# Optimization experiments

Hardware: AMD Instinct MI355X
Metric: run time of the kernel (lower is better)

Reference implementation:

```python
import jax, jax.numpy as jnp
import numpy as np

FREQ_DIM = 64
BLOCK_DIM = 64
N = 256          # lattice sites
CH = 6           # channel_num -> block diagonals at offsets -1, 0, +1
S = 2 * 16 + CH - 2   # seq_num = 36
BS = 4           # block_size (kron of two 2x2 matrices)
HID = 128
EPS = 1e-5
B = 32

_e = np.eye(2)
_sx = np.array([[0., 1.], [1., 0.]])
_siy = np.array([[0., 1.], [-1., 0.]])
_sz = np.array([[1., 0.], [0., -1.]])
_p = [_e, _sx, _siy, _sz]
KRONS = jnp.asarray(np.stack([np.kron(_p[a], _p[b]) for a in range(4) for b in range(4)]).astype(np.float32))  # (16,4,4)
Z1 = KRONS[12]  # kron(sigma_z, I) used for interaction blocks ('z1')


def _bn(h, g, b):
    # BatchNorm1d in training mode: biased batch statistics over axis 0
    mu = h.mean(axis=0)
    v = h.var(axis=0)
    return g * (h - mu) / jnp.sqrt(v + EPS) + b


def _mlp(x, Win, bin_, Wmid, bmid, Wout, bout, gamma, beta):
    # depth-4 MLP: Lin+ReLU, then (BN,Lin,ReLU) x2, then BN,Lin,ReLU
    h = jax.nn.relu(x @ Win + bin_)
    for i in range(Wmid.shape[0]):
        h = jax.nn.relu(_bn(h, gamma[i], beta[i]) @ Wmid[i] + bmid[i])
    return jax.nn.relu(_bn(h, gamma[-1], beta[-1]) @ Wout + bout)


def _lstm(xs, h0, c0, Wih, Whh, bih, bhh):
    # xs: (B, T, S); torch gate order i, f, g, o
    def step(carry, x_t):
        h, c = carry
        gates = x_t @ Wih.T + h @ Whh.T + (bih + bhh)
        i, f, g, o = jnp.split(gates, 4, axis=-1)
        c = jax.nn.sigmoid(f) * c + jax.nn.sigmoid(i) * jnp.tanh(g)
        h = jax.nn.sigmoid(o) * jnp.tanh(c)
        return (h, c), h
    _, hs = jax.lax.scan(step, (h0, c0), jnp.swapaxes(xs, 0, 1))
    return jnp.swapaxes(hs, 0, 1)


def setup_inputs() -> dict:
    key = jax.random.key(0)
    ks = iter(jax.random.split(key, 48))
    def w(shape, s=0.05):
        return jax.random.normal(next(ks), shape, dtype=jnp.float32) * s
    d = {
        'x': w((B, FREQ_DIM + BLOCK_DIM), 1.0),
        'fd_Win': w((FREQ_DIM, HID)), 'fd_bin': w((HID,)),
        'fd_Wmid': w((2, HID, HID)), 'fd_bmid': w((2, HID)),
        'fd_Wout': w((HID, S)), 'fd_bout': w((S,)),
        'fd_gamma': jnp.ones((3, HID), jnp.float32), 'fd_beta': jnp.zeros((3, HID), jnp.float32),
        'bd_Win': w((BLOCK_DIM, HID)), 'bd_bin': w((HID,)),
        'bd_Wmid': w((2, HID, HID)), 'bd_bmid': w((2, HID)),
        'bd_Wout': w((HID, S)), 'bd_bout': w((S,)),
        'bd_gamma': jnp.ones((3, HID), jnp.float32), 'bd_beta': jnp.zeros((3, HID), jnp.float32),
        'sc_Win': w((S, 1, HID)), 'sc_bin': w((S, HID)),
        'sc_Wmid': w((S, 2, HID, HID)), 'sc_bmid': w((S, 2, HID)),
        'sc_Wout': w((S, HID, N)), 'sc_bout': w((S, N)),
        'sc_gamma': jnp.ones((S, 3, HID), jnp.float32), 'sc_beta': jnp.zeros((S, 3, HID), jnp.float32),
        'lstm_Wih': w((4 * S, S)), 'lstm_Whh': w((4 * S, S)),
        'lstm_bih': w((4 * S,)), 'lstm_bhh': w((4 * S,)),
        'mix_W': w((S, 2 * S)), 'mix_b': w((S,)),
    }
    return d


def reference(x, fd_Win, fd_bin, fd_Wmid, fd_bmid, fd_Wout, fd_bout, fd_gamma, fd_beta,
              bd_Win, bd_bin, bd_Wmid, bd_bmid, bd_Wout, bd_bout, bd_gamma, bd_beta,
              sc_Win, sc_bin, sc_Wmid, sc_bmid, sc_Wout, sc_bout, sc_gamma, sc_beta,
              lstm_Wih, lstm_Whh, lstm_bih, lstm_bhh, mix_W, mix_b):
    Bsz = x.shape[0]
    block = _mlp(x[:, FREQ_DIM:], bd_Win, bd_bin, bd_Wmid, bd_bmid, bd_Wout, bd_bout, bd_gamma, bd_beta)  # (B,S)
    freq = _mlp(x[:, :FREQ_DIM], fd_Win, fd_bin, fd_Wmid, fd_bmid, fd_Wout, fd_bout, fd_gamma, fd_beta)   # (B,S)
    # S independent scalar->N MLPs, batched with vmap over the stacked params
    sc = jax.vmap(_mlp)(freq.T[:, :, None], sc_Win, sc_bin, sc_Wmid, sc_bmid,
                        sc_Wout, sc_bout, sc_gamma, sc_beta)  # (S,B,N)
    freq_seq = jnp.cos(sc).transpose(1, 2, 0)   # (B,N,S)
    seq = _lstm(freq_seq, block, jnp.zeros_like(block), lstm_Wih, lstm_Whh, lstm_bih, lstm_bhh)  # (B,N,S)
    block_seq = jnp.concatenate([jnp.broadcast_to(block[:, :, None], (Bsz, S, N)),
                                 jnp.swapaxes(seq, 1, 2)], axis=1)  # (B,2S,N)
    # 1x1 Conv2d == channel mixing matmul
    mixed = jnp.einsum('bcn,oc->bon', block_seq, mix_W) + mix_b[None, :, None]  # (B,S,N)
    inter = mixed[:, :CH - 2]                          # (B,CH-2,N)
    onsite = mixed[:, CH - 2:].reshape(Bsz, 2, 16, N)  # (B,2,16,N)
    H_int = jnp.einsum('bcn,ij->bcnij', inter, Z1)         # (B,CH-2,N,4,4)
    H_os = jnp.einsum('bgkn,kij->bgnij', onsite, KRONS)    # (B,2,N,4,4) summed over 16 pairs
    half = (CH - 2) // 2
    strips = jnp.concatenate([H_int[:, :half], H_os, H_int[:, half:]], axis=1)  # (B,CH,N,4,4)
    strips = strips.reshape(Bsz, CH // 2, 2, N, BS, BS)
    # banded block assembly: strip i lives on block-diagonal offset i - (CH//2)//2
    grid = jnp.zeros((Bsz, 2, N, N, BS, BS), dtype=x.dtype)
    for i in range(CH // 2):
        o = i - (CH // 2) // 2
        rows = jnp.arange(N - abs(o)) + max(0, -o)
        cols = rows + o
        grid = grid.at[:, :, rows, cols].set(strips[:, i][:, :, rows])
    matrix = grid.transpose(0, 1, 2, 4, 3, 5).reshape(Bsz, 2, N * BS, N * BS)
    return matrix
```

## Files before the change

kernel.cpp:

```cpp
#include <hip/hip_runtime.h>
#include <math.h>

#define EPSF 1e-5f
typedef __attribute__((ext_vector_type(2))) float f32x2;
typedef __attribute__((ext_vector_type(4))) float f32x4;

__device__ __forceinline__ float sigf(float x) { return 1.f / (1.f + __expf(-x)); }
__device__ __forceinline__ float tanhf_fast(float x) { return 1.f - 2.f / (__expf(2.f * x) + 1.f); }
__device__ __forceinline__ float rdlane(float v, int k) {
    return __int_as_float(__builtin_amdgcn_readlane(__float_as_int(v), k));
}

__device__ __forceinline__ float pauliv(int p, int r, int c) {
    switch (p) {
        case 0: return (r == c) ? 1.f : 0.f;
        case 1: return (r != c) ? 1.f : 0.f;
        case 2: return (r == 0 && c == 1) ? 1.f : ((r == 1 && c == 0) ? -1.f : 0.f);
        default: return (r == c) ? ((r == 0) ? 1.f : -1.f) : 0.f;
    }
}

__device__ void mlp64_body(const float* __restrict__ xin,
                           const float* __restrict__ Win,
                           const float* __restrict__ bin_,
                           const float* __restrict__ Wmid,
                           const float* __restrict__ bmid,
                           const float* __restrict__ Wout,
                           const float* __restrict__ bout,
                           const float* __restrict__ gamma,
                           const float* __restrict__ beta,
                           float* __restrict__ out)
{
    __shared__ float sX[2048];
    __shared__ float sA[4096];
    __shared__ float sB[4096];
    __shared__ float sMu[128], sRs[128];
    int tid = threadIdx.x;

    for (int idx = tid; idx < 2048; idx += 1024) {
        int b = idx >> 6, c = idx & 63;
        sX[idx] = xin[b * 128 + c];
    }
    __syncthreads();

    for (int idx = tid; idx < 4096; idx += 1024) {
        int b = idx >> 7, j = idx & 127;
        float acc = bin_[j];
        for (int c = 0; c < 64; ++c) acc = fmaf(sX[b * 64 + c], Win[c * 128 + j], acc);
        sA[idx] = fmaxf(acc, 0.f);
    }
    __syncthreads();

    float* cur = sA;
    float* nxt = sB;
    for (int l = 0; l < 3; ++l) {
        if (tid < 128) {
            float s = 0.f, s2 = 0.f;
            for (int b = 0; b < 32; ++b) {
                float v = cur[b * 128 + tid];
                s += v; s2 += v * v;
            }
            float mu = s * (1.f / 32.f);
            float var = s2 * (1.f / 32.f) - mu * mu;
            sMu[tid] = mu;
            sRs[tid] = rsqrtf(var + EPSF);
        }
        __syncthreads();
        for (int idx = tid; idx < 4096; idx += 1024) {
            int j = idx & 127;
            cur[idx] = gamma[l * 128 + j] * (cur[idx] - sMu[j]) * sRs[j] + beta[l * 128 + j];
        }
        __syncthreads();
        if (l < 2) {
            for (int idx = tid; idx < 4096; idx += 1024) {
                int b = idx >> 7, j = idx & 127;
                float acc = bmid[l * 128 + j];
                for (int c = 0; c < 128; ++c)
                    acc = fmaf(cur[b * 128 + c], Wmid[(l * 128 + c) * 128 + j], acc);
                nxt[idx] = fmaxf(acc, 0.f);
            }
            __syncthreads();
            float* t = cur; cur = nxt; nxt = t;
        } else {
            for (int idx = tid; idx < 1152; idx += 1024) {
                int b = idx / 36, j = idx - b * 36;
                float acc = bout[j];
                for (int c = 0; c < 128; ++c)
                    acc = fmaf(cur[b * 128 + c], Wout[c * 36 + j], acc);
                out[idx] = fmaxf(acc, 0.f);
            }
        }
    }
}

__global__ __launch_bounds__(1024) void k_mlp2(
    const float* __restrict__ x,
    const float* fdWin, const float* fdbin, const float* fdWmid, const float* fdbmid,
    const float* fdWout, const float* fdbout, const float* fdg, const float* fdbt,
    const float* bdWin, const float* bdbin, const float* bdWmid, const float* bdbmid,
    const float* bdWout, const float* bdbout, const float* bdg, const float* bdbt,
    float* freq, float* blk)
{
    if (blockIdx.x == 0)
        mlp64_body(x + 64, bdWin, bdbin, bdWmid, bdbmid, bdWout, bdbout, bdg, bdbt, blk);
    else
        mlp64_body(x, fdWin, fdbin, fdWmid, fdbmid, fdWout, fdbout, fdg, fdbt, freq);
}

__global__ __launch_bounds__(512) void k_sc1(
    const float* __restrict__ freq,
    const float* __restrict__ Win,
    const float* __restrict__ bin_,
    const float* __restrict__ Wmid,
    const float* __restrict__ bmid,
    const float* __restrict__ gamma,
    const float* __restrict__ beta,
    float* __restrict__ actW)
{
    int s = blockIdx.x, tid = threadIdx.x;
    __shared__ float sA[4096];
    __shared__ float sB[4096];
    __shared__ float sMu[128], sRs[128];
    const float* Wm = Wmid + (size_t)s * 2 * 128 * 128;
    const float* gm = gamma + s * 3 * 128;
    const float* bt = beta + s * 3 * 128;

    for (int idx = tid; idx < 4096; idx += 512) {
        int b = idx >> 7, j = idx & 127;
        float acc = fmaf(freq[b * 36 + s], Win[s * 128 + j], bin_[s * 128 + j]);
        sA[idx] = fmaxf(acc, 0.f);
    }
    __syncthreads();

    float* cur = sA;
    float* nxt = sB;
    for (int l = 0; l < 3; ++l) {
        if (tid < 128) {
            float sm = 0.f, s2 = 0.f;
            for (int b = 0; b < 32; ++b) {
                float v = cur[b * 128 + tid];
                sm += v; s2 += v * v;
            }
            float mu = sm * (1.f / 32.f);
            float var = s2 * (1.f / 32.f) - mu * mu;
            sMu[tid] = mu;
            sRs[tid] = rsqrtf(var + EPSF);
        }
        __syncthreads();
        for (int idx = tid; idx < 4096; idx += 512) {
            int j = idx & 127;
            cur[idx] = gm[l * 128 + j] * (cur[idx] - sMu[j]) * sRs[j] + bt[l * 128 + j];
        }
        __syncthreads();
        if (l < 2) {
            int jj = tid & 127, bb = tid >> 7;
            float acc[8];
            #pragma unroll
            for (int k = 0; k < 8; ++k) acc[k] = bmid[(s * 2 + l) * 128 + jj];
            for (int c = 0; c < 128; ++c) {
                float w = Wm[(l * 128 + c) * 128 + jj];
                #pragma unroll
                for (int k = 0; k < 8; ++k)
                    acc[k] = fmaf(cur[(bb + 4 * k) * 128 + c], w, acc[k]);
            }
            __syncthreads();
            #pragma unroll
            for (int k = 0; k < 8; ++k) nxt[(bb + 4 * k) * 128 + jj] = fmaxf(acc[k], 0.f);
            __syncthreads();
            float* t = cur; cur = nxt; nxt = t;
        } else {
            for (int idx = tid; idx < 4096; idx += 512)
                actW[(size_t)s * 4096 + idx] = cur[idx];
        }
    }
}

__global__ __launch_bounds__(512) void k_sc2(
    const float* __restrict__ actW,
    const float* __restrict__ Wout,
    const float* __restrict__ bout,
    float* __restrict__ fseq2)
{
    int bidx = blockIdx.x;
    int s = bidx >> 2, q = bidx & 3;
    int tid = threadIdx.x;
    __shared__ float sAct[4096];
    for (int idx = tid; idx < 4096; idx += 512)
        sAct[idx] = actW[(size_t)s * 4096 + idx];
    __syncthreads();

    int nn = (tid & 63) + q * 64;
    int bb = tid >> 6;
    const float* Wo = Wout + (size_t)s * 128 * 256;
    float acc[4];
    #pragma unroll
    for (int k = 0; k < 4; ++k) acc[k] = bout[s * 256 + nn];
    #pragma unroll 4
    for (int c = 0; c < 128; ++c) {
        float w = Wo[c * 256 + nn];
        #pragma unroll
        for (int k = 0; k < 4; ++k)
            acc[k] = fmaf(sAct[(bb + 8 * k) * 128 + c], w, acc[k]);
    }
    #pragma unroll
    for (int k = 0; k < 4; ++k) {
        float v = fmaxf(acc[k], 0.f);
        fseq2[((size_t)s * 32 + bb + 8 * k) * 256 + nn] = __cosf(v);
    }
}

__global__ __launch_bounds__(512) void k_xg(
    const float* __restrict__ fseq2, const float* __restrict__ Wih,
    const float* __restrict__ bih, const float* __restrict__ bhh,
    float* __restrict__ Xg)
{
    int t = blockIdx.x, tid = threadIdx.x;
    __shared__ float sF[1152];
    __shared__ float sWt[36 * 144];
    for (int idx = tid; idx < 1152; idx += 512) {
        int s = idx >> 5, b = idx & 31;
        sF[b * 36 + s] = fseq2[(size_t)idx * 256 + t];
    }
    for (int idx = tid; idx < 5184; idx += 512) {
        int j = idx / 36, s = idx - j * 36;
        sWt[s * 144 + j] = Wih[idx];
    }
    __syncthreads();
    for (int idx = tid; idx < 4608; idx += 512) {
        int b = idx / 144, j = idx - b * 144;
        int g = j / 36, u = j - g * 36;
        float acc = bih[j] + bhh[j];
        #pragma unroll
        for (int s = 0; s < 36; ++s)
            acc = fmaf(sF[b * 36 + s], sWt[s * 144 + j], acc);
        Xg[(((size_t)b * 256 + t) * 36 + u) * 4 + g] = acc;
    }
}

#define PF 8
#define NZBLK 4032
__global__ __launch_bounds__(128) void k_lstm_zero(
    const float* __restrict__ Xg,
    const float* __restrict__ blk,
    const float* __restrict__ Whh,
    float* __restrict__ hseq2,
    float* __restrict__ out, long total4)
{
    __shared__ float hbuf[256 * 36];
    __shared__ f32x2 sEx[2][2][40];

    if (blockIdx.x >= 32) {
        f32x4* o = (f32x4*)out;
        f32x4 z = f32x4{0.f, 0.f, 0.f, 0.f};
        long start = (long)(blockIdx.x - 32) * 128 + threadIdx.x;
        long stride = (long)NZBLK * 128;
        for (long i = start; i < total4; i += stride) o[i] = z;
        return;
    }

    int b = blockIdx.x;
    int wid = threadIdx.x >> 6;
    int lane = threadIdx.x & 63;
    int uu = lane < 36 ? lane : 35;
    bool active = lane < 36;

    f32x2 w2[36];
    {
        const float* wA = Whh + (size_t)(wid * 72 + uu) * 36;
        const float* wB = Whh + (size_t)(wid * 72 + 36 + uu) * 36;
        #pragma unroll
        for (int k = 0; k < 36; ++k) w2[k] = f32x2{wA[k], wB[k]};
    }

    float hv = blk[b * 36 + uu];
    float c = 0.f;
    const f32x2* xb2 = (const f32x2*)(Xg + (size_t)b * 256 * 144);

    f32x2 pipe[PF];
    #pragma unroll
    for (int i = 0; i < PF; ++i) pipe[i] = xb2[(i * 36 + uu) * 2 + wid];

    #pragma unroll 8
    for (int t = 0; t < 256; ++t) {
        f32x2 acc0 = pipe[t & (PF - 1)];
        if (t + PF < 256) pipe[t & (PF - 1)] = xb2[((t + PF) * 36 + uu) * 2 + wid];

        f32x2 acc1 = f32x2{0.f, 0.f}, acc2 = f32x2{0.f, 0.f}, acc3 = f32x2{0.f, 0.f};
        #pragma unroll
        for (int k = 0; k < 36; k += 4) {
            float h0 = rdlane(hv, k),     h1 = rdlane(hv, k + 1);
            float h2 = rdlane(hv, k + 2), h3 = rdlane(hv, k + 3);
            acc0 = __builtin_elementwise_fma(w2[k],     f32x2{h0, h0}, acc0);
            acc1 = __builtin_elementwise_fma(w2[k + 1], f32x2{h1, h1}, acc1);
            acc2 = __builtin_elementwise_fma(w2[k + 2], f32x2{h2, h2}, acc2);
            acc3 = __builtin_elementwise_fma(w2[k + 3], f32x2{h3, h3}, acc3);
        }
        f32x2 a = (acc0 + acc1) + (acc2 + acc3);

        f32x2 mypair;
        if (wid == 0) mypair = f32x2{sigf(a.x), sigf(a.y)};
        else          mypair = f32x2{tanhf_fast(a.x), sigf(a.y)};
        if (active) sEx[t & 1][wid][uu] = mypair;
        __syncthreads();
        f32x2 other = sEx[t & 1][wid ^ 1][uu];
        f32x2 ivfv = (wid == 0) ? mypair : other;
        f32x2 gvov = (wid == 0) ? other : mypair;
        c = fmaf(ivfv.y, c, ivfv.x * gvov.x);
        hv = gvov.y * tanhf_fast(c);
        if (wid == 0 && active) hbuf[t * 36 + uu] = hv;
    }

    __syncthreads();
    {
        f32x4* dst = (f32x4*)(hseq2 + (size_t)b * 256 * 36);
        const f32x4* src = (const f32x4*)hbuf;
        for (int i = threadIdx.x; i < 2304; i += 128) dst[i] = src[i];
    }
}

__global__ __launch_bounds__(256) void k_mixed(
    const float* __restrict__ blk, const float* __restrict__ hseq2,
    const float* __restrict__ mixW, const float* __restrict__ mixb,
    float* __restrict__ mixed)
{
    int bq = blockIdx.x;
    int b = bq >> 2, oq = bq & 3;
    int tid = threadIdx.x;
    __shared__ float sH[256 * 37];
    __shared__ float sW[9 * 36];
    __shared__ float sBase[9];
    for (int idx = tid; idx < 9216; idx += 256) {
        int t = idx / 36, u = idx - t * 36;
        sH[t * 37 + u] = hseq2[(size_t)b * 9216 + idx];
    }
    for (int idx = tid; idx < 9 * 36; idx += 256) {
        int o = idx / 36, u = idx - o * 36;
        sW[idx] = mixW[(oq * 9 + o) * 72 + 36 + u];
    }
    if (tid < 9) {
        int o = oq * 9 + tid;
        float acc = mixb[o];
        for (int c = 0; c < 36; ++c) acc = fmaf(mixW[o * 72 + c], blk[b * 36 + c], acc);
        sBase[tid] = acc;
    }
    __syncthreads();
    int n = tid;
    #pragma unroll
    for (int o = 0; o < 9; ++o) {
        float acc = sBase[o];
        #pragma unroll
        for (int u = 0; u < 36; ++u)
            acc = fmaf(sW[o * 36 + u], sH[n * 37 + u], acc);
        mixed[((size_t)b * 36 + oq * 9 + o) * 256 + n] = acc;
    }
}

__global__ __launch_bounds__(256) void k_sparse(
    const float* __restrict__ mixed, float* __restrict__ out)
{
    int bg = blockIdx.x;
    int g = bg & 1, b = bg >> 1;
    int n = threadIdx.x;
    const float* mb = mixed + (size_t)b * 36 * 256;
    float vSub = mb[(size_t)g * 256 + n];
    float vSup = mb[(size_t)(2 + g) * 256 + n];
    float ch[16];
    #pragma unroll
    for (int k = 0; k < 16; ++k) ch[k] = mb[(size_t)(4 + 16 * g + k) * 256 + n];
    float d[16];
    #pragma unroll
    for (int e = 0; e < 16; ++e) {
        int r = e >> 2, cc = e & 3;
        float acc = 0.f;
        #pragma unroll
        for (int k = 0; k < 16; ++k) {
            float kv = pauliv(k >> 2, r >> 1, cc >> 1) * pauliv(k & 3, r & 1, cc & 1);
            if (kv == 1.f) acc = acc + ch[k];
            else if (kv == -1.f) acc = acc - ch[k];
        }
        d[e] = acc;
    }

    float* base = out + (size_t)bg * 1024 * 1024;
    #pragma unroll
    for (int r = 0; r < 4; ++r)
        *(f32x4*)(base + (size_t)(4 * n + r) * 1024 + 4 * n) =
            f32x4{d[r * 4 + 0], d[r * 4 + 1], d[r * 4 + 2], d[r * 4 + 3]};
    if (n > 0) {
        #pragma unroll
        for (int r = 0; r < 4; ++r)
            base[(size_t)(4 * n + r) * 1024 + 4 * (n - 1) + r] = (r < 2) ? vSub : -vSub;
    }
    if (n < 255) {
        #pragma unroll
        for (int r = 0; r < 4; ++r)
            base[(size_t)(4 * n + r) * 1024 + 4 * (n + 1) + r] = (r < 2) ? vSup : -vSup;
    }
}

extern "C" void kernel_launch(void* const* d_in, const int* in_sizes, int n_in,
                              void* d_out, int out_size, void* d_ws, size_t ws_size,
                              hipStream_t stream) {
    const float* x      = (const float*)d_in[0];
    const float* fdWin  = (const float*)d_in[1];
    const float* fdbin  = (const float*)d_in[2];
    const float* fdWmid = (const float*)d_in[3];
    const float* fdbmid = (const float*)d_in[4];
    const float* fdWout = (const float*)d_in[5];
    const float* fdbout = (const float*)d_in[6];
    const float* fdg    = (const float*)d_in[7];
    const float* fdbt   = (const float*)d_in[8];
    const float* bdWin  = (const float*)d_in[9];
    const float* bdbin  = (const float*)d_in[10];
    const float* bdWmid = (const float*)d_in[11];
    const float* bdbmid = (const float*)d_in[12];
    const float* bdWout = (const float*)d_in[13];
    const float* bdbout = (const float*)d_in[14];
    const float* bdg    = (const float*)d_in[15];
    const float* bdbt   = (const float*)d_in[16];
    const float* scWin  = (const float*)d_in[17];
    const float* scbin  = (const float*)d_in[18];
    const float* scWmid = (const float*)d_in[19];
    const float* scbmid = (const float*)d_in[20];
    const float* scWout = (const float*)d_in[21];
    const float* scbout = (const float*)d_in[22];
    const float* scg    = (const float*)d_in[23];
    const float* scbt   = (const float*)d_in[24];
    const float* Wih    = (const float*)d_in[25];
    const float* Whh    = (const float*)d_in[26];
    const float* bih    = (const float*)d_in[27];
    const float* bhh    = (const float*)d_in[28];
    const float* mixW   = (const float*)d_in[29];
    const float* mixb   = (const float*)d_in[30];

    float* ws    = (float*)d_ws;
    float* freq  = ws;
    float* blk   = ws + 1152;
    float* fseq2 = ws + 2304;
    float* Xg    = ws + 297216;
    float* hseq2 = ws + 1476864;
    float* mixed = ws + 1771776;
    float* actW  = Xg;

    float* out = (float*)d_out;
    long total4 = (long)out_size / 4;

    k_mlp2<<<2, 1024, 0, stream>>>(x,
        fdWin, fdbin, fdWmid, fdbmid, fdWout, fdbout, fdg, fdbt,
        bdWin, bdbin, bdWmid, bdbmid, bdWout, bdbout, bdg, bdbt,
        freq, blk);
    k_sc1<<<36, 512, 0, stream>>>(freq, scWin, scbin, scWmid, scbmid, scg, scbt, actW);
    k_sc2<<<144, 512, 0, stream>>>(actW, scWout, scbout, fseq2);
    k_xg<<<256, 512, 0, stream>>>(fseq2, Wih, bih, bhh, Xg);
    k_lstm_zero<<<32 + NZBLK, 128, 0, stream>>>(Xg, blk, Whh, hseq2, out, total4);
    k_mixed<<<128, 256, 0, stream>>>(blk, hseq2, mixW, mixb, mixed);
    k_sparse<<<64, 256, 0, stream>>>(mixed, out);
}
```

Measured before the change: 327.6 us.

## Move output zero-fill into MLP kernel and add spinning heater blocks beside LSTM

The large output zero-fill is moved from the LSTM kernel into the first MLP kernel, which now launches many extra blocks that overlap the fill with the two MLP blocks. The LSTM kernel's extra blocks instead run dummy FMA loops until an atomic counter shows all 32 recurrence blocks have finished, presumably to keep the GPU clocks or busy state elevated during the latency-bound recurrence. A flag is reset in the xg kernel to coordinate this. This adds wasted compute and power, and the zero-fill now competes with the MLP rather than hiding behind the LSTM.

```diff
diff --git a/kernel.cpp b/kernel.cpp
--- a/kernel.cpp
+++ b/kernel.cpp
@@ -93,14 +93,22 @@
     }
 }
 
-__global__ __launch_bounds__(1024) void k_mlp2(
+__global__ __launch_bounds__(1024) void k_mlp2_zero(
     const float* __restrict__ x,
     const float* fdWin, const float* fdbin, const float* fdWmid, const float* fdbmid,
     const float* fdWout, const float* fdbout, const float* fdg, const float* fdbt,
     const float* bdWin, const float* bdbin, const float* bdWmid, const float* bdbmid,
     const float* bdWout, const float* bdbout, const float* bdg, const float* bdbt,
-    float* freq, float* blk)
-{
+    float* freq, float* blk, float* out, long total4)
+{
+    if (blockIdx.x >= 2) {
+        f32x4* o = (f32x4*)out;
+        f32x4 z = f32x4{0.f, 0.f, 0.f, 0.f};
+        long start = (long)(blockIdx.x - 2) * 1024 + threadIdx.x;
+        long stride = (long)2046 * 1024;
+        for (long i = start; i < total4; i += stride) o[i] = z;
+        return;
+    }
     if (blockIdx.x == 0)
         mlp64_body(x + 64, bdWin, bdbin, bdWmid, bdbmid, bdWout, bdbout, bdg, bdbt, blk);
     else
@@ -212,8 +220,9 @@
 __global__ __launch_bounds__(512) void k_xg(
     const float* __restrict__ fseq2, const float* __restrict__ Wih,
     const float* __restrict__ bih, const float* __restrict__ bhh,
-    float* __restrict__ Xg)
-{
+    float* __restrict__ Xg, int* __restrict__ flag)
+{
+    if (blockIdx.x == 0 && threadIdx.x == 0) *flag = 0;
     int t = blockIdx.x, tid = threadIdx.x;
     __shared__ float sF[1152];
     __shared__ float sWt[36 * 144];
@@ -238,23 +247,30 @@
 }
 
 #define PF 8
-#define NZBLK 4032
-__global__ __launch_bounds__(128) void k_lstm_zero(
+__global__ __launch_bounds__(128) void k_lstm_heat(
     const float* __restrict__ Xg,
     const float* __restrict__ blk,
     const float* __restrict__ Whh,
     float* __restrict__ hseq2,
-    float* __restrict__ out, long total4)
+    int* __restrict__ flag)
 {
     __shared__ float hbuf[256 * 36];
     __shared__ f32x2 sEx[2][2][40];
 
     if (blockIdx.x >= 32) {
-        f32x4* o = (f32x4*)out;
-        f32x4 z = f32x4{0.f, 0.f, 0.f, 0.f};
-        long start = (long)(blockIdx.x - 32) * 128 + threadIdx.x;
-        long stride = (long)NZBLK * 128;
-        for (long i = start; i < total4; i += stride) o[i] = z;
+        float a0 = 1.0f + threadIdx.x, a1 = 1.1f, a2 = 1.2f, a3 = 1.3f;
+        for (int it = 0; it < 2000; ++it) {
+            #pragma unroll
+            for (int j = 0; j < 128; ++j) {
+                a0 = fmaf(a0, 0.9999f, 0.0001f);
+                a1 = fmaf(a1, 0.9999f, 0.0002f);
+                a2 = fmaf(a2, 0.9999f, 0.0003f);
+                a3 = fmaf(a3, 0.9999f, 0.0004f);
+            }
+            if (__hip_atomic_load(flag, __ATOMIC_RELAXED, __HIP_MEMORY_SCOPE_AGENT) >= 32)
+                break;
+        }
+        asm volatile("" :: "v"(a0), "v"(a1), "v"(a2), "v"(a3));
         return;
     }
 
@@ -316,6 +332,8 @@
         const f32x4* src = (const f32x4*)hbuf;
         for (int i = threadIdx.x; i < 2304; i += 128) dst[i] = src[i];
     }
+    if (threadIdx.x == 0)
+        __hip_atomic_fetch_add(flag, 1, __ATOMIC_RELAXED, __HIP_MEMORY_SCOPE_AGENT);
 }
 
 __global__ __launch_bounds__(256) void k_mixed(
@@ -441,18 +459,19 @@
     float* hseq2 = ws + 1476864;
     float* mixed = ws + 1771776;
     float* actW  = Xg;
+    int*   flag  = (int*)(ws + 2066688);
 
     float* out = (float*)d_out;
     long total4 = (long)out_size / 4;
 
-    k_mlp2<<<2, 1024, 0, stream>>>(x,
+    k_mlp2_zero<<<2048, 1024, 0, stream>>>(x,
         fdWin, fdbin, fdWmid, fdbmid, fdWout, fdbout, fdg, fdbt,
         bdWin, bdbin, bdWmid, bdbmid, bdWout, bdbout, bdg, bdbt,
-        freq, blk);
+        freq, blk, out, total4);
     k_sc1<<<36, 512, 0, stream>>>(freq, scWin, scbin, scWmid, scbmid, scg, scbt, actW);
     k_sc2<<<144, 512, 0, stream>>>(actW, scWout, scbout, fseq2);
-    k_xg<<<256, 512, 0, stream>>>(fseq2, Wih, bih, bhh, Xg);
-    k_lstm_zero<<<32 + NZBLK, 128, 0, stream>>>(Xg, blk, Whh, hseq2, out, total4);
+    k_xg<<<256, 512, 0, stream>>>(fseq2, Wih, bih, bhh, Xg, flag);
+    k_lstm_heat<<<255, 128, 0, stream>>>(Xg, blk, Whh, hseq2, flag);
     k_mixed<<<128, 256, 0, stream>>>(blk, hseq2, mixW, mixb, mixed);
     k_sparse<<<64, 256, 0, stream>>>(mixed, out);
 }
```

Measured after the change: 321.7 us. About the same (-1.8%).
